# Kernel tuning notes

Hardware: AMD Instinct MI355X
Metric: run time of the kernel (lower is better)

## Reference

```python
import jax, jax.numpy as jnp
import numpy as np

B, TAU, T0V, D, PD, RD, DO, K = 2048, 32, 96, 64, 3, 1, 64, 16
R = 1.0  # radius for radius_graph


def setup_inputs() -> dict:
    key = jax.random.key(0)
    ks = jax.random.split(key, 9)
    return {
        "x": jax.random.normal(ks[0], (B, TAU, D), jnp.float32),
        "pos": jax.random.uniform(ks[1], (B, TAU, PD), jnp.float32),
        "rot": jax.random.uniform(ks[2], (B, TAU, RD), jnp.float32),
        "old_x": jax.random.normal(ks[3], (B, 128, D), jnp.float32),
        "old_pos": jax.random.uniform(ks[4], (B, 128, PD), jnp.float32),
        "old_rot": jax.random.uniform(ks[5], (B, 128, RD), jnp.float32),
        "W_self": jax.random.normal(ks[6], (D + PD + RD, DO), jnp.float32) * 0.1,
        "W_nbr": jax.random.normal(ks[7], (D + PD + RD, DO), jnp.float32) * 0.1,
        "bias": jax.random.normal(ks[8], (DO,), jnp.float32) * 0.1,
        "T0": T0V,
        "tau": TAU,
    }


def reference(x, pos, rot, old_x, old_pos, old_rot, W_self, W_nbr, bias, T0, tau):
    # --- update(): scatter new observations into the state buffers ---
    # (regular case: T[b]=T0, taus[b]=tau for all b, so new_idx is a static slice)
    new_x = old_x.at[:, T0:T0 + tau].set(x)
    new_pos = old_pos.at[:, T0:T0 + tau].set(pos)
    new_rot = old_rot.at[:, T0:T0 + tau].set(rot)

    L = T0 + tau  # valid (non-padded) nodes per env
    nx, npv, nr = new_x[:, :L], new_pos[:, :L], new_rot[:, :L]
    h = jnp.concatenate([nx, npv, nr], axis=-1)  # [B, L, D+PD+RD] node features

    # --- radius_graph(r, max_num_neighbors=K, loop=True) + remove_noncausal_edges ---
    # edge (j -> i) kept iff ||pos_j - pos_i|| <= r and j < i (causal, drops self-loops)
    diff = npv[:, :, None, :] - npv[:, None, :, :]           # [B, L, L, PD]
    d2 = jnp.sum(diff * diff, axis=-1)                        # [B, L, L] (target i, source j)
    t_idx = jnp.arange(L)
    causal = t_idx[None, :] < t_idx[:, None]                  # [L, L] j < i
    mask = causal[None, :, :] & (d2 <= R * R)
    masked_d2 = jnp.where(mask, d2, jnp.inf)
    neg_d, nbr_idx = jax.lax.top_k(-masked_d2, K)             # k nearest causal in-radius
    valid = jnp.isfinite(neg_d)                               # [B, L, K]

    # --- gnn(): one message-passing layer (stand-in for external gnn) ---
    msg = h @ W_nbr                                           # [B, L, DO]
    gathered = jax.vmap(lambda m, i: m[i])(msg, nbr_idx)      # [B, L, K, DO]
    agg = jnp.sum(gathered * valid[..., None].astype(msg.dtype), axis=2)
    out = jax.nn.relu(h @ W_self + agg + bias)                # [B, L, DO]

    # --- gather flat_new_idx / scatter into padded output ---
    padded_output = out[:, T0:T0 + tau]                       # [B, tau, DO]
    return padded_output, new_x, new_pos, new_rot
```

## Files before the change

### kernel.cpp

```cpp
#include <hip/hip_runtime.h>
#include <hip/hip_bf16.h>
#include <cstdint>
#include <cstddef>

#define NB 2048
#define TAU 32
#define T0C 96
#define LQ 128
#define DD 64
#define DOUT 64
#define KK 16

typedef unsigned long long u64;
typedef __attribute__((ext_vector_type(8))) short short8;
typedef __attribute__((ext_vector_type(4))) float f32x4;

#define KINV 1e30

__device__ __forceinline__ float fmul_exact(float a, float b) {
  float r; asm("v_mul_f32 %0, %1, %2" : "=v"(r) : "v"(a), "v"(b)); return r;
}
__device__ __forceinline__ float fadd_exact(float a, float b) {
  float r; asm("v_add_f32 %0, %1, %2" : "=v"(r) : "v"(a), "v"(b)); return r;
}
__device__ __forceinline__ unsigned short f2bf(float f) {
  __hip_bfloat16 h = __float2bfloat16(f);
  return *reinterpret_cast<unsigned short*>(&h);
}
__device__ __forceinline__ double shfl_xor_f64(double v, int mask) {
  u64 u = __double_as_longlong(v);
  int lo = __shfl_xor((int)(unsigned)(u & 0xffffffffULL), mask, 64);
  int hi = __shfl_xor((int)(unsigned)(u >> 32), mask, 64);
  return __longlong_as_double(((u64)(unsigned)hi << 32) | (unsigned)lo);
}

#define CA(i, j) { double _lo = fmin(kd[i], kd[j]); double _hi = fmax(kd[i], kd[j]); kd[i] = _lo; kd[j] = _hi; }
#define CD(i, j) { double _lo = fmin(kd[i], kd[j]); double _hi = fmax(kd[i], kd[j]); kd[i] = _hi; kd[j] = _lo; }

#define SORT16() do { \
  CA(0,1)  CD(2,3)  CA(4,5)  CD(6,7)  CA(8,9)  CD(10,11) CA(12,13) CD(14,15) \
  CA(0,2)  CA(1,3)  CD(4,6)  CD(5,7)  CA(8,10) CA(9,11)  CD(12,14) CD(13,15) \
  CA(0,1)  CA(2,3)  CD(4,5)  CD(6,7)  CA(8,9)  CA(10,11) CD(12,13) CD(14,15) \
  CA(0,4)  CA(1,5)  CA(2,6)  CA(3,7)  CD(8,12) CD(9,13)  CD(10,14) CD(11,15) \
  CA(0,2)  CA(1,3)  CA(4,6)  CA(5,7)  CD(8,10) CD(9,11)  CD(12,14) CD(13,15) \
  CA(0,1)  CA(2,3)  CA(4,5)  CA(6,7)  CD(8,9)  CD(10,11) CD(12,13) CD(14,15) \
  CA(0,8)  CA(1,9)  CA(2,10) CA(3,11) CA(4,12) CA(5,13)  CA(6,14)  CA(7,15)  \
  CA(0,4)  CA(1,5)  CA(2,6)  CA(3,7)  CA(8,12) CA(9,13)  CA(10,14) CA(11,15) \
  CA(0,2)  CA(1,3)  CA(4,6)  CA(5,7)  CA(8,10) CA(9,11)  CA(12,14) CA(13,15) \
  CA(0,1)  CA(2,3)  CA(4,5)  CA(6,7)  CA(8,9)  CA(10,11) CA(12,13) CA(14,15) \
} while (0)

#define MERGE16() do { \
  CA(0,8)  CA(1,9)  CA(2,10) CA(3,11) CA(4,12) CA(5,13)  CA(6,14)  CA(7,15)  \
  CA(0,4)  CA(1,5)  CA(2,6)  CA(3,7)  CA(8,12) CA(9,13)  CA(10,14) CA(11,15) \
  CA(0,2)  CA(1,3)  CA(4,6)  CA(5,7)  CA(8,10) CA(9,11)  CA(12,14) CA(13,15) \
  CA(0,1)  CA(2,3)  CA(4,5)  CA(6,7)  CA(8,9)  CA(10,11) CA(12,13) CA(14,15) \
} while (0)

#define SHUF_MERGE(mask) do { \
  double pb[16]; \
  _Pragma("unroll") \
  for (int _i = 0; _i < 16; ++_i) pb[_i] = shfl_xor_f64(kd[15 - _i], mask); \
  _Pragma("unroll") \
  for (int _i = 0; _i < 16; ++_i) kd[_i] = fmin(kd[_i], pb[_i]); \
  MERGE16(); \
} while (0)

__global__ __launch_bounds__(256, 4) void navgcm_fused(
    const float* __restrict__ x, const float* __restrict__ pos_in, const float* __restrict__ rot_in,
    const float* __restrict__ old_x, const float* __restrict__ old_pos, const float* __restrict__ old_rot,
    const float* __restrict__ W_self, const float* __restrict__ W_nbr, const float* __restrict__ bias,
    float* __restrict__ outp)
{
  const int b = blockIdx.x;
  const int tid = threadIdx.x;
  const int lane = tid & 63;
  const int wv = tid >> 6;
  const int fr = lane & 15;
  const int fg = lane >> 4;

  __shared__ __align__(16) unsigned char uni[36864];
  __shared__ float px[LQ], py[LQ], pz[LQ], rt[LQ];
  __shared__ uint4 selidx[32];

  unsigned short (*Hs)[72]  = reinterpret_cast<unsigned short(*)[72]>(uni);
  unsigned short (*Wn)[72]  = reinterpret_cast<unsigned short(*)[72]>(uni + 18432);
  unsigned short (*Wsf)[72] = reinterpret_cast<unsigned short(*)[72]>(uni + 27648);
  float (*msgs)[66] = reinterpret_cast<float(*)[66]>(uni);

  float4* dnx = (float4*)(outp + (size_t)NB * TAU * DOUT);
  #pragma unroll
  for (int it = 0; it < 8; ++it) {
    int n = tid + 256 * it;
    int row = n >> 4, c4 = n & 15;
    const float4* src = (row < T0C)
        ? (const float4*)(old_x + ((size_t)b * LQ + row) * DD)
        : (const float4*)(x + ((size_t)b * TAU + (row - T0C)) * DD);
    float4 v = src[c4];
    dnx[(size_t)b * 2048 + n] = v;
    ushort4 w4;
    w4.x = f2bf(v.x); w4.y = f2bf(v.y); w4.z = f2bf(v.z); w4.w = f2bf(v.w);
    *reinterpret_cast<ushort4*>(&Hs[row][c4 * 4]) = w4;
  }

  #pragma unroll
  for (int it = 0; it < 8; ++it) {
    int m = tid + 256 * it;
    int n = m & 63, kp = m >> 6;
    float a0 = W_nbr[(2 * kp) * DOUT + n], a1 = W_nbr[(2 * kp + 1) * DOUT + n];
    *reinterpret_cast<uint32_t*>(&Wn[n][2 * kp]) =
        (uint32_t)f2bf(a0) | ((uint32_t)f2bf(a1) << 16);
    float s0 = W_self[(2 * kp) * DOUT + n], s1 = W_self[(2 * kp + 1) * DOUT + n];
    *reinterpret_cast<uint32_t*>(&Wsf[n][2 * kp]) =
        (uint32_t)f2bf(s0) | ((uint32_t)f2bf(s1) << 16);
  }

  float* dpos = outp + (size_t)NB * TAU * DOUT + (size_t)NB * LQ * DD;
  float* drot = dpos + (size_t)NB * LQ * 3;
  if (tid < LQ) {
    int t = tid;
    float p0, p1, p2, rr;
    if (t < T0C) {
      const float* s = old_pos + ((size_t)b * LQ + t) * 3;
      p0 = s[0]; p1 = s[1]; p2 = s[2];
      rr = old_rot[(size_t)b * LQ + t];
    } else {
      const float* s = pos_in + ((size_t)b * TAU + (t - T0C)) * 3;
      p0 = s[0]; p1 = s[1]; p2 = s[2];
      rr = rot_in[(size_t)b * TAU + (t - T0C)];
    }
    px[t] = p0; py[t] = p1; pz[t] = p2; rt[t] = rr;
    size_t g = (size_t)b * LQ + t;
    dpos[g * 3 + 0] = p0; dpos[g * 3 + 1] = p1; dpos[g * 3 + 2] = p2;
    drot[g] = rr;
  }
  __syncthreads();

  {
    const int q = tid >> 3, s8 = tid & 7;
    const int i = T0C + q;
    const float pix = px[i], piy = py[i], piz = pz[i];
    double kd[16];
    #pragma unroll
    for (int c = 0; c < 16; ++c) {
      int j = 8 * c + s8;
      float dx = pix - px[j], dy = piy - py[j], dz = piz - pz[j];
      float d2 = fadd_exact(fadd_exact(fmul_exact(dx, dx), fmul_exact(dy, dy)),
                            fmul_exact(dz, dz));
      bool valid = (d2 <= 1.0f) && (j < i);
      double key = fma((double)__float_as_uint(d2), 128.0, (double)j);
      kd[c] = valid ? key : KINV;
    }
    SORT16();
    SHUF_MERGE(1);
    SHUF_MERGE(2);
    SHUF_MERGE(4);

    if (s8 == 0) {
      uint32_t w[4] = {0u, 0u, 0u, 0u};
      #pragma unroll
      for (int t = 0; t < KK; ++t) {
        double kv = kd[t];
        uint32_t jj;
        if (kv >= 1e29) {
          jj = 127u;
        } else {
          uint32_t d2b = (uint32_t)(kv * 0.0078125);
          double rem = kv - 128.0 * (double)d2b;
          jj = (uint32_t)rem;
        }
        w[t >> 2] |= jj << ((t & 3) * 8);
      }
      uint4 sv; sv.x = w[0]; sv.y = w[1]; sv.z = w[2]; sv.w = w[3];
      selidx[q] = sv;
    }
  }

  short8 bW[4][2];
  #pragma unroll
  for (int nt = 0; nt < 4; ++nt)
    #pragma unroll
    for (int ks = 0; ks < 2; ++ks)
      bW[nt][ks] = *reinterpret_cast<const short8*>(&Wn[nt * 16 + fr][ks * 32 + fg * 8]);

  f32x4 acc[2][4];
  #pragma unroll
  for (int m = 0; m < 2; ++m)
    #pragma unroll
    for (int n = 0; n < 4; ++n)
      acc[m][n] = (f32x4){0.f, 0.f, 0.f, 0.f};

  #pragma unroll
  for (int mtl = 0; mtl < 2; ++mtl) {
    int mrow = (2 * wv + mtl) * 16;
    short8 a0 = *reinterpret_cast<const short8*>(&Hs[mrow + fr][fg * 8]);
    short8 a1 = *reinterpret_cast<const short8*>(&Hs[mrow + fr][32 + fg * 8]);
    #pragma unroll
    for (int nt = 0; nt < 4; ++nt) {
      acc[mtl][nt] = __builtin_amdgcn_mfma_f32_16x16x32_bf16(a0, bW[nt][0], acc[mtl][nt], 0, 0, 0);
      acc[mtl][nt] = __builtin_amdgcn_mfma_f32_16x16x32_bf16(a1, bW[nt][1], acc[mtl][nt], 0, 0, 0);
    }
  }

  const int mt = wv & 1;
  const int ntb = (wv >> 1) * 2;
  short8 aQ0 = *reinterpret_cast<const short8*>(&Hs[T0C + mt * 16 + fr][fg * 8]);
  short8 aQ1 = *reinterpret_cast<const short8*>(&Hs[T0C + mt * 16 + fr][32 + fg * 8]);
  f32x4 acc2[2];
  #pragma unroll
  for (int n = 0; n < 2; ++n) acc2[n] = (f32x4){0.f, 0.f, 0.f, 0.f};
  #pragma unroll
  for (int ntl = 0; ntl < 2; ++ntl) {
    int nt = ntb + ntl;
    short8 b0 = *reinterpret_cast<const short8*>(&Wsf[nt * 16 + fr][fg * 8]);
    short8 b1 = *reinterpret_cast<const short8*>(&Wsf[nt * 16 + fr][32 + fg * 8]);
    acc2[ntl] = __builtin_amdgcn_mfma_f32_16x16x32_bf16(aQ0, b0, acc2[ntl], 0, 0, 0);
    acc2[ntl] = __builtin_amdgcn_mfma_f32_16x16x32_bf16(aQ1, b1, acc2[ntl], 0, 0, 0);
  }
  __syncthreads();

  float wn4[4][4];
  #pragma unroll
  for (int nt = 0; nt < 4; ++nt) {
    int col = nt * 16 + fr;
    wn4[nt][0] = W_nbr[64 * DOUT + col];
    wn4[nt][1] = W_nbr[65 * DOUT + col];
    wn4[nt][2] = W_nbr[66 * DOUT + col];
    wn4[nt][3] = W_nbr[67 * DOUT + col];
  }
  #pragma unroll
  for (int mtl = 0; mtl < 2; ++mtl) {
    #pragma unroll
    for (int r = 0; r < 4; ++r) {
      int row = (2 * wv + mtl) * 16 + fg * 4 + r;
      float p0 = px[row], p1 = py[row], p2 = pz[row], p3 = rt[row];
      #pragma unroll
      for (int nt = 0; nt < 4; ++nt) {
        float v = acc[mtl][nt][r]
                + p0 * wn4[nt][0] + p1 * wn4[nt][1] + p2 * wn4[nt][2] + p3 * wn4[nt][3];
        msgs[row][nt * 16 + fr] = (row == LQ - 1) ? 0.f : v;
      }
    }
  }
  __syncthreads();

  #pragma unroll
  for (int ntl = 0; ntl < 2; ++ntl) {
    int col = (ntb + ntl) * 16 + fr;
    float ws0 = W_self[64 * DOUT + col], ws1 = W_self[65 * DOUT + col];
    float ws2 = W_self[66 * DOUT + col], ws3 = W_self[67 * DOUT + col];
    float bi = bias[col];
    #pragma unroll
    for (int r = 0; r < 4; ++r) {
      int q = mt * 16 + fg * 4 + r;
      int row = T0C + q;
      uint4 sv = selidx[q];
      float agg = 0.f;
      #pragma unroll
      for (int s = 0; s < KK; ++s) {
        uint32_t wd = (s < 4) ? sv.x : (s < 8) ? sv.y : (s < 12) ? sv.z : sv.w;
        int j = (wd >> ((s & 3) * 8)) & 0xff;
        agg += msgs[j][col];
      }
      float v = acc2[ntl][r] + agg + bi
              + px[row] * ws0 + py[row] * ws1 + pz[row] * ws2 + rt[row] * ws3;
      v = fmaxf(v, 0.f);
      outp[((size_t)b * TAU + q) * DOUT + col] = v;
    }
  }
}

extern "C" void kernel_launch(void* const* d_in, const int* in_sizes, int n_in,
                              void* d_out, int out_size, void* d_ws, size_t ws_size,
                              hipStream_t stream) {
  (void)in_sizes; (void)n_in; (void)d_ws; (void)ws_size; (void)out_size;
  const float* x       = (const float*)d_in[0];
  const float* pos     = (const float*)d_in[1];
  const float* rot     = (const float*)d_in[2];
  const float* old_x   = (const float*)d_in[3];
  const float* old_pos = (const float*)d_in[4];
  const float* old_rot = (const float*)d_in[5];
  const float* W_self  = (const float*)d_in[6];
  const float* W_nbr   = (const float*)d_in[7];
  const float* bias    = (const float*)d_in[8];
  float* out = (float*)d_out;

  hipLaunchKernelGGL(navgcm_fused, dim3(NB), dim3(256), 0, stream,
                     x, pos, rot, old_x, old_pos, old_rot, W_self, W_nbr, bias, out);
}
```

Measured before the change: 45.92 us.

## Pre-transpose weights to bf16 in a prep kernel, store messages as bf16

A small pre-kernel converts W_nbr and W_self to transposed bf16 in the workspace once per call. The main kernel then loads MFMA B-operands straight from global memory instead of having every block transpose and convert the weights into LDS. The message buffer is stored as bf16 rather than fp32, which halves shared memory use and lets occupancy be raised to 6 blocks per CU. The trade-offs are an extra kernel launch, uncached global loads of the weight fragments, and lower precision in the aggregated messages.

Measured after the change: 51.18 us. +11.4%, slower.

```diff
diff --git a/kernel.cpp b/kernel.cpp
--- a/kernel.cpp
+++ b/kernel.cpp
@@ -66,10 +66,21 @@
   MERGE16(); \
 } while (0)
 
-__global__ __launch_bounds__(256, 4) void navgcm_fused(
+__global__ __launch_bounds__(256) void prep_w(
+    const float* __restrict__ W_nbr, const float* __restrict__ W_self,
+    unsigned short* __restrict__ wst) {
+  int idx = blockIdx.x * 256 + threadIdx.x;
+  int m = idx & 4095;
+  int n = m >> 6, k = m & 63;
+  const float* src = (idx < 4096) ? W_nbr : W_self;
+  wst[idx] = f2bf(src[k * DOUT + n]);
+}
+
+__global__ __launch_bounds__(256, 6) void navgcm_fused(
     const float* __restrict__ x, const float* __restrict__ pos_in, const float* __restrict__ rot_in,
     const float* __restrict__ old_x, const float* __restrict__ old_pos, const float* __restrict__ old_rot,
     const float* __restrict__ W_self, const float* __restrict__ W_nbr, const float* __restrict__ bias,
+    const unsigned short* __restrict__ wst,
     float* __restrict__ outp)
 {
   const int b = blockIdx.x;
@@ -79,14 +90,12 @@
   const int fr = lane & 15;
   const int fg = lane >> 4;
 
-  __shared__ __align__(16) unsigned char uni[36864];
+  __shared__ __align__(16) unsigned char uni[18432];
   __shared__ float px[LQ], py[LQ], pz[LQ], rt[LQ];
   __shared__ uint4 selidx[32];
 
-  unsigned short (*Hs)[72]  = reinterpret_cast<unsigned short(*)[72]>(uni);
-  unsigned short (*Wn)[72]  = reinterpret_cast<unsigned short(*)[72]>(uni + 18432);
-  unsigned short (*Wsf)[72] = reinterpret_cast<unsigned short(*)[72]>(uni + 27648);
-  float (*msgs)[66] = reinterpret_cast<float(*)[66]>(uni);
+  unsigned short (*Hs)[72] = reinterpret_cast<unsigned short(*)[72]>(uni);
+  unsigned short (*msgs)[68] = reinterpret_cast<unsigned short(*)[68]>(uni);
 
   float4* dnx = (float4*)(outp + (size_t)NB * TAU * DOUT);
   #pragma unroll
@@ -101,18 +110,6 @@
     ushort4 w4;
     w4.x = f2bf(v.x); w4.y = f2bf(v.y); w4.z = f2bf(v.z); w4.w = f2bf(v.w);
     *reinterpret_cast<ushort4*>(&Hs[row][c4 * 4]) = w4;
-  }
-
-  #pragma unroll
-  for (int it = 0; it < 8; ++it) {
-    int m = tid + 256 * it;
-    int n = m & 63, kp = m >> 6;
-    float a0 = W_nbr[(2 * kp) * DOUT + n], a1 = W_nbr[(2 * kp + 1) * DOUT + n];
-    *reinterpret_cast<uint32_t*>(&Wn[n][2 * kp]) =
-        (uint32_t)f2bf(a0) | ((uint32_t)f2bf(a1) << 16);
-    float s0 = W_self[(2 * kp) * DOUT + n], s1 = W_self[(2 * kp + 1) * DOUT + n];
-    *reinterpret_cast<uint32_t*>(&Wsf[n][2 * kp]) =
-        (uint32_t)f2bf(s0) | ((uint32_t)f2bf(s1) << 16);
   }
 
   float* dpos = outp + (size_t)NB * TAU * DOUT + (size_t)NB * LQ * DD;
@@ -176,12 +173,15 @@
     }
   }
 
+  const unsigned short* wn_t = wst;
+  const unsigned short* ws_t = wst + 4096;
+
   short8 bW[4][2];
   #pragma unroll
   for (int nt = 0; nt < 4; ++nt)
     #pragma unroll
     for (int ks = 0; ks < 2; ++ks)
-      bW[nt][ks] = *reinterpret_cast<const short8*>(&Wn[nt * 16 + fr][ks * 32 + fg * 8]);
+      bW[nt][ks] = *reinterpret_cast<const short8*>(&wn_t[(nt * 16 + fr) * 64 + ks * 32 + fg * 8]);
 
   f32x4 acc[2][4];
   #pragma unroll
@@ -212,8 +212,8 @@
   #pragma unroll
   for (int ntl = 0; ntl < 2; ++ntl) {
     int nt = ntb + ntl;
-    short8 b0 = *reinterpret_cast<const short8*>(&Wsf[nt * 16 + fr][fg * 8]);
-    short8 b1 = *reinterpret_cast<const short8*>(&Wsf[nt * 16 + fr][32 + fg * 8]);
+    short8 b0 = *reinterpret_cast<const short8*>(&ws_t[(nt * 16 + fr) * 64 + fg * 8]);
+    short8 b1 = *reinterpret_cast<const short8*>(&ws_t[(nt * 16 + fr) * 64 + 32 + fg * 8]);
     acc2[ntl] = __builtin_amdgcn_mfma_f32_16x16x32_bf16(aQ0, b0, acc2[ntl], 0, 0, 0);
     acc2[ntl] = __builtin_amdgcn_mfma_f32_16x16x32_bf16(aQ1, b1, acc2[ntl], 0, 0, 0);
   }
@@ -238,7 +238,7 @@
       for (int nt = 0; nt < 4; ++nt) {
         float v = acc[mtl][nt][r]
                 + p0 * wn4[nt][0] + p1 * wn4[nt][1] + p2 * wn4[nt][2] + p3 * wn4[nt][3];
-        msgs[row][nt * 16 + fr] = (row == LQ - 1) ? 0.f : v;
+        msgs[row][nt * 16 + fr] = (row == LQ - 1) ? (unsigned short)0 : f2bf(v);
       }
     }
   }
@@ -260,7 +260,8 @@
       for (int s = 0; s < KK; ++s) {
         uint32_t wd = (s < 4) ? sv.x : (s < 8) ? sv.y : (s < 12) ? sv.z : sv.w;
         int j = (wd >> ((s & 3) * 8)) & 0xff;
-        agg += msgs[j][col];
+        unsigned short mv = msgs[j][col];
+        agg += __uint_as_float((uint32_t)mv << 16);
       }
       float v = acc2[ntl][r] + agg + bi
               + px[row] * ws0 + py[row] * ws1 + pz[row] * ws2 + rt[row] * ws3;
@@ -273,7 +274,7 @@
 extern "C" void kernel_launch(void* const* d_in, const int* in_sizes, int n_in,
                               void* d_out, int out_size, void* d_ws, size_t ws_size,
                               hipStream_t stream) {
-  (void)in_sizes; (void)n_in; (void)d_ws; (void)ws_size; (void)out_size;
+  (void)in_sizes; (void)n_in; (void)ws_size; (void)out_size;
   const float* x       = (const float*)d_in[0];
   const float* pos     = (const float*)d_in[1];
   const float* rot     = (const float*)d_in[2];
@@ -284,7 +285,9 @@
   const float* W_nbr   = (const float*)d_in[7];
   const float* bias    = (const float*)d_in[8];
   float* out = (float*)d_out;
-
+  unsigned short* wst = (unsigned short*)d_ws;
+
+  hipLaunchKernelGGL(prep_w, dim3(32), dim3(256), 0, stream, W_nbr, W_self, wst);
   hipLaunchKernelGGL(navgcm_fused, dim3(NB), dim3(256), 0, stream,
-                     x, pos, rot, old_x, old_pos, old_rot, W_self, W_nbr, bias, out);
-}
+                     x, pos, rot, old_x, old_pos, old_rot, W_self, W_nbr, bias, wst, out);
+}
```
